# Performance work log

Measured on AMD Instinct MI355X. Metric: run time of the kernel, lower is better.

Reference implementation:

```python
import jax, jax.numpy as jnp
import numpy as np

B, C, N, K = 2, 128, 8192, 16
DL = 128  # dim_L; Fourier half-dim = 64; mlp hidden = 32


def setup_inputs() -> dict:
    key = jax.random.key(0)
    ks = jax.random.split(key, 16)
    s = 0.05
    return {
        "x": jax.random.normal(ks[0], (B, C, N, 1), jnp.float32),
        "coords": jax.random.normal(ks[1], (B, N, 4), jnp.float32),
        "idx": jax.random.randint(ks[2], (B, N, K), 0, N, jnp.int64),
        "B_gauss": jax.random.normal(ks[3], (4, DL // 2), jnp.float32),
        "W1": jax.random.normal(ks[4], (DL, DL // 4), jnp.float32) * s,
        "b1": jax.random.normal(ks[5], (DL // 4,), jnp.float32) * s,
        "W2": jax.random.normal(ks[6], (DL // 4, C), jnp.float32) * s,
        "b2": jax.random.normal(ks[7], (C,), jnp.float32) * s,
        "Wq": jax.random.normal(ks[8], (C, C), jnp.float32) * s,
        "bq": jax.random.normal(ks[9], (C,), jnp.float32) * s,
        "Wk": jax.random.normal(ks[10], (C, C), jnp.float32) * s,
        "bk": jax.random.normal(ks[11], (C,), jnp.float32) * s,
        "Wv": jax.random.normal(ks[12], (C, C), jnp.float32) * s,
        "bv": jax.random.normal(ks[13], (C,), jnp.float32) * s,
        "Wo": jax.random.normal(ks[14], (C, C), jnp.float32) * s,
        "bo": jax.random.normal(ks[15], (C,), jnp.float32) * s,
    }


def reference(x, coords, idx, B_gauss, W1, b1, W2, b2, Wq, bq, Wk, bk, Wv, bv, Wo, bo):
    xs = x[..., 0]  # [B, C, N]
    # gather neighbor coords/features via KNN idx (vmapped over batch)
    nb_coords = jax.vmap(lambda c, i: c[i])(coords, idx)          # [B, N, K, 4]
    nb_feats = jax.vmap(lambda f, i: f[:, i])(xs, idx)            # [B, C, N, K]
    delta_p = nb_coords - coords[:, :, None, :]                   # [B, N, K, 4]
    # random-Fourier geometric embedding
    proj = jnp.matmul(delta_p, B_gauss)                           # [B, N, K, DL/2]
    two_pi = 2.0 * jnp.pi
    E_freq = jnp.concatenate([jnp.sin(two_pi * proj), jnp.cos(two_pi * proj)], axis=-1)
    h = jax.nn.relu(E_freq @ W1 + b1) @ W2 + b2                   # [B, N, K, C]
    E_geo = jnp.transpose(h, (0, 3, 1, 2))                        # [B, C, N, K]
    # 1x1 conv projections == channel matmuls (PyTorch conv weight acts as out<-in)
    Q = jnp.einsum('oc,bcn->bon', Wq, xs) + bq[None, :, None]     # [B, C, N]
    KV_in = nb_feats + E_geo                                      # [B, C, N, K]
    Kt = jnp.einsum('oc,bcnk->bonk', Wk, KV_in) + bk[None, :, None, None]
    Vt = jnp.einsum('oc,bcnk->bonk', Wv, KV_in) + bv[None, :, None, None]
    # local dot-product attention over K neighbors
    attn = jnp.sum(Q[..., None] * Kt, axis=1, keepdims=True) / jnp.sqrt(jnp.float32(C))
    attn = jax.nn.softmax(attn, axis=-1)                          # [B, 1, N, K]
    out = jnp.sum(attn * Vt, axis=-1, keepdims=True)              # [B, C, N, 1]
    out = jnp.einsum('oc,bcnk->bonk', Wo, out) + bo[None, :, None, None]
    return out
```

## Files before the change

kernel.cpp:

```cpp
#include <hip/hip_runtime.h>


using u16 = unsigned short;
using u32 = unsigned int;
using u64 = unsigned long long;

typedef short bf16x8 __attribute__((ext_vector_type(8)));
typedef float f32x4  __attribute__((ext_vector_type(4)));

__device__ __forceinline__ float bl(u32 u) { return __uint_as_float(u << 16); }
__device__ __forceinline__ float bh(u32 u) { return __uint_as_float(u & 0xffff0000u); }
__device__ __forceinline__ float b2f(u16 u) { return __uint_as_float(((u32)u) << 16); }
__device__ __forceinline__ u16 f2b(float f) {
    u32 u = __float_as_uint(f);
    u32 r = u + 0x7fffu + ((u >> 16) & 1u);
    return (u16)(r >> 16);
}
__device__ __forceinline__ u64 pack4(float a, float b, float c, float d) {
    return (u64)f2b(a) | ((u64)f2b(b) << 16) | ((u64)f2b(c) << 32) | ((u64)f2b(d) << 48);
}
__device__ __forceinline__ int fidxA(int m, int c) {
    return (((m >> 4)*4 + (c >> 5))*64 + ((c >> 3) & 3)*16 + (m & 15))*8 + (c & 7);
}

__global__ void __launch_bounds__(512)
k_pt(const float* __restrict__ x,
     const float* __restrict__ Wq, const float* __restrict__ bq,
     const float* __restrict__ Wk,
     const float* __restrict__ Wv, const float* __restrict__ bv,
     const float* __restrict__ Wo, const float* __restrict__ bo,
     const float* __restrict__ W1, const float* __restrict__ W2,
     u16* __restrict__ Afrag, u16* __restrict__ Wovfrag,
     u16* __restrict__ W1frag, u16* __restrict__ W2frag,
     u16* __restrict__ Wow2frag,
     float* __restrict__ bA, float* __restrict__ bov,
     u16* __restrict__ xT)
{
    const int blk = blockIdx.x, tid = threadIdx.x;

    if (blk >= 130) {
        __shared__ u16 tile[32][33];
        const int blk2 = blk - 130;
        const int b  = blk2 >> 10;
        const int ct = (blk2 >> 8) & 3;
        const int nt = blk2 & 255;
        const int tx = tid & 31, ty = tid >> 5;
        const size_t xb = (size_t)b * 128 * 8192;
        #pragma unroll
        for (int j = 0; j < 2; ++j) {
            int c = ct*32 + ty + j*16;
            tile[ty + j*16][tx] = f2b(x[xb + (size_t)c * 8192 + (size_t)(nt*32 + tx)]);
        }
        __syncthreads();
        #pragma unroll
        for (int j = 0; j < 2; ++j) {
            int n = nt*32 + ty + j*16;
            xT[xb + (size_t)n * 128 + (size_t)(ct*32 + tx)] = tile[tx][ty + j*16];
        }
        return;
    }

    const int i = tid & 127, p = tid >> 7;
    if (blk < 128) {
        __shared__ float sWk[128], sWo[128];
        __shared__ float s_pA[4][128], s_pV[4][128];
        __shared__ float sWovRow[128];
        __shared__ float s_p2[32][17];
        if (tid < 128) sWk[tid] = Wk[tid*128 + blk];
        else if (tid < 256) sWo[tid-128] = Wo[blk*128 + (tid-128)];
        __syncthreads();
        float accA = 0.f, accV = 0.f;
        #pragma unroll 8
        for (int o = p*32; o < p*32 + 32; ++o) {
            accA += sWk[o] * Wq[o*128 + i];
            accV += sWo[o] * Wv[o*128 + i];
        }
        s_pA[p][i] = accA; s_pV[p][i] = accV;
        __syncthreads();
        if (tid < 128) {
            float v = s_pA[0][tid] + s_pA[1][tid] + s_pA[2][tid] + s_pA[3][tid];
            Afrag[fidxA(blk, tid)] = f2b(v);
        } else if (tid < 256) {
            int ii = tid - 128;
            float v = s_pV[0][ii] + s_pV[1][ii] + s_pV[2][ii] + s_pV[3][ii];
            Wovfrag[fidxA(blk, ii)] = f2b(v);
            sWovRow[ii] = v;
        }
        __syncthreads();
        {
            int h = tid >> 4, sub = tid & 15;
            float a = 0.f;
            #pragma unroll
            for (int jj = 0; jj < 8; ++jj)
                a += sWovRow[sub*8 + jj] * W2[h*128 + sub*8 + jj];
            s_p2[h][sub] = a;
        }
        __syncthreads();
        if (tid < 32) {
            float v = 0.f;
            #pragma unroll
            for (int s = 0; s < 16; ++s) v += s_p2[tid][s];
            Wow2frag[(((blk >> 4)*64 + (tid >> 3)*16 + (blk & 15)))*8 + (tid & 7)] = f2b(v);
        }
    } else if (blk == 128) {
        __shared__ float s_r[2][4][128];
        float a1 = 0.f, a3 = 0.f;
        #pragma unroll 8
        for (int o = p*32; o < p*32 + 32; ++o) {
            a1 += Wk[o*128 + i] * bq[o];
            a3 += Wo[i*128 + o] * bv[o];
        }
        s_r[0][p][i] = a1; s_r[1][p][i] = a3;
        __syncthreads();
        if (tid < 128) {
            bA[tid] = s_r[0][0][tid] + s_r[0][1][tid] + s_r[0][2][tid] + s_r[0][3][tid];
        } else if (tid < 256) {
            int ii = tid - 128;
            bov[ii] = s_r[1][0][ii] + s_r[1][1][ii] + s_r[1][2][ii] + s_r[1][3][ii] + bo[ii];
        }
    } else {
        for (int e = tid; e < 4096; e += 512) {
            int ii = e & 127, r2 = e >> 7;
            {
                int nt = r2 >> 4, lmm = r2 & 15;
                int ks = ii >> 5, q = (ii >> 3) & 3, j = ii & 7;
                W1frag[((nt*4 + ks)*64 + q*16 + lmm)*8 + j] = f2b(W1[ii*32 + r2]);
            }
            {
                int mt = r2 >> 4, lmm = r2 & 15;
                int ks = ii >> 5, q = (ii >> 3) & 3, j = ii & 7;
                W2frag[((mt*4 + ks)*64 + q*16 + lmm)*8 + j] = f2b(W2[r2*128 + ii]);
            }
        }
    }
}

__global__ void __launch_bounds__(256, 2)
k_main(const u16* __restrict__ xT, const float* __restrict__ coords,
       const int* __restrict__ idx, const float* __restrict__ Bg,
       const float* __restrict__ b1g, const float* __restrict__ b2g,
       const u16* __restrict__ Afrag, const u16* __restrict__ Wovfrag,
       const u16* __restrict__ W1frag, const u16* __restrict__ W2frag,
       const u16* __restrict__ Wow2frag,
       const float* __restrict__ bAg, const float* __restrict__ bovg,
       float* __restrict__ out)
{
    __shared__ __align__(16) u16   sH[128][40];
    __shared__ __align__(16) u16   s_qkb[8][136];
    __shared__ __align__(16) u16   s_gb[8][40];
    __shared__ __align__(16) u16   s_xbb[8][136];
    __shared__ __align__(16) float s_del[128][4];
    __shared__ float s_attn[8][17];
    __shared__ u16   sHbar[32][12];
    __shared__ __align__(16) float s_b2[128];
    __shared__ float s_bov[128], s_b1[32];
    __shared__ __align__(16) float sBgT[64][4];
    __shared__ int s_idx[128];

    const int tid = threadIdx.x;
    const int w = tid >> 6, l = tid & 63, lm = l & 15, lq = l >> 4, lmm = lm & 7;
    const int g0 = blockIdx.x * 8;
    const int bsel = g0 >> 13;
    const int n0 = g0 & 8191;
    const size_t bbase = ((size_t)bsel) << 13;
    const float inv_sqrtC = 0.08838834764831845f;

    if (tid < 128) { s_bov[tid] = bovg[tid]; s_b2[tid] = b2g[tid]; }
    else if (tid < 160) { s_b1[tid-128] = b1g[tid-128]; }
    sBgT[tid >> 2][tid & 3] = Bg[(tid & 3)*64 + (tid >> 2)];

    if (tid < 128) {
        int j = idx[(size_t)g0*16 + tid];
        s_idx[tid] = j;
        float4 cj = *(const float4*)&coords[(size_t)(bbase + j)*4];
        float4 cn = *(const float4*)&coords[(size_t)(g0 + (tid >> 4))*4];
        *(float4*)s_del[tid] = make_float4(cj.x-cn.x, cj.y-cn.y, cj.z-cn.z, cj.w-cn.w);
    }
    {
        f32x4 accq[2] = {{0.f,0.f,0.f,0.f},{0.f,0.f,0.f,0.f}};
        const bf16x8* Af = (const bf16x8*)Afrag;
        bf16x8 bfr[4];
        #pragma unroll
        for (int ks = 0; ks < 4; ++ks)
            bfr[ks] = *(const bf16x8*)&xT[(((size_t)(g0 + lmm)) << 7) + ks*32 + lq*8];
        #pragma unroll
        for (int mi = 0; mi < 2; ++mi) {
            const int ct = w*2 + mi;
            #pragma unroll
            for (int ks = 0; ks < 4; ++ks) {
                bf16x8 a = Af[(ct*4 + ks)*64 + l];
                accq[mi] = __builtin_amdgcn_mfma_f32_16x16x32_bf16(a, bfr[ks], accq[mi], 0, 0, 0);
            }
        }
        if (lm < 8) {
            #pragma unroll
            for (int mi = 0; mi < 2; ++mi) {
                int c0 = (w*2 + mi)*16 + lq*4;
                float4 ba4 = *(const float4*)&bAg[c0];
                *(u64*)&s_qkb[lm][c0] = pack4(accq[mi][0] + ba4.x, accq[mi][1] + ba4.y,
                                              accq[mi][2] + ba4.z, accq[mi][3] + ba4.w);
            }
        }
    }
    __syncthreads();

    {
        const bf16x8* W1f = (const bf16x8*)W1frag;
        bf16x8 w1f[2][4];
        #pragma unroll
        for (int nt = 0; nt < 2; ++nt)
            #pragma unroll
            for (int ks = 0; ks < 4; ++ks) w1f[nt][ks] = W1f[(nt*4 + ks)*64 + l];
        #pragma unroll
        for (int mi = 0; mi < 2; ++mi) {
            const int mt = w*2 + mi;
            float4 d = *(const float4*)s_del[mt*16 + lm];
            bf16x8 ea[4];
            #pragma unroll
            for (int ksp = 0; ksp < 2; ++ksp) {
                #pragma unroll
                for (int jp = 0; jp < 4; ++jp) {
                    int f = ksp*32 + lq*8 + jp*2;
                    float4 ga = *(const float4*)sBgT[f];
                    float4 gb = *(const float4*)sBgT[f+1];
                    float p0 = d.x*ga.x + d.y*ga.y + d.z*ga.z + d.w*ga.w;
                    float p1 = d.x*gb.x + d.y*gb.y + d.z*gb.z + d.w*gb.w;
                    p0 -= floorf(p0); p1 -= floorf(p1);
                    ((u32*)&ea[ksp])[jp]   = (u32)f2b(__builtin_amdgcn_sinf(p0))
                                           | ((u32)f2b(__builtin_amdgcn_sinf(p1)) << 16);
                    ((u32*)&ea[ksp+2])[jp] = (u32)f2b(__builtin_amdgcn_cosf(p0))
                                           | ((u32)f2b(__builtin_amdgcn_cosf(p1)) << 16);
                }
            }
            f32x4 acch[2] = {{0.f,0.f,0.f,0.f},{0.f,0.f,0.f,0.f}};
            #pragma unroll
            for (int ks = 0; ks < 4; ++ks) {
                acch[0] = __builtin_amdgcn_mfma_f32_16x16x32_bf16(ea[ks], w1f[0][ks], acch[0], 0,0,0);
                acch[1] = __builtin_amdgcn_mfma_f32_16x16x32_bf16(ea[ks], w1f[1][ks], acch[1], 0,0,0);
            }
            #pragma unroll
            for (int nt = 0; nt < 2; ++nt) {
                float b1v = s_b1[nt*16 + lm];
                #pragma unroll
                for (int r = 0; r < 4; ++r)
                    sH[mt*16 + lq*4 + r][nt*16 + lm] = f2b(fmaxf(acch[nt][r] + b1v, 0.f));
            }
        }
    }
    if (w < 2) {
        const bf16x8* W2f = (const bf16x8*)W2frag;
        f32x4 accg = {0.f,0.f,0.f,0.f};
        #pragma unroll
        for (int ks = 0; ks < 4; ++ks) {
            bf16x8 a = W2f[(w*4 + ks)*64 + l];
            bf16x8 bv = *(const bf16x8*)&s_qkb[lmm][ks*32 + lq*8];
            accg = __builtin_amdgcn_mfma_f32_16x16x32_bf16(a, bv, accg, 0, 0, 0);
        }
        if (lm < 8) {
            int m0 = w*16 + lq*4;
            *(u64*)&s_gb[lm][m0] = pack4(accg[0], accg[1], accg[2], accg[3]);
        }
    }
    __syncthreads();

    {
        bf16x8 xnb[2][4];
        const size_t rb0 = ((size_t)(bbase + s_idx[(w*2 + 0)*16 + lm])) << 7;
        const size_t rb1 = ((size_t)(bbase + s_idx[(w*2 + 1)*16 + lm])) << 7;
        #pragma unroll
        for (int ks = 0; ks < 4; ++ks)
            xnb[0][ks] = *(const bf16x8*)&xT[rb0 + ks*32 + lq*8];
        #pragma unroll
        for (int ks = 0; ks < 4; ++ks)
            xnb[1][ks] = *(const bf16x8*)&xT[rb1 + ks*32 + lq*8];
        bf16x8 bq4[5];
        #pragma unroll
        for (int ks = 0; ks < 4; ++ks) bq4[ks] = *(const bf16x8*)&s_qkb[lmm][ks*32 + lq*8];
        bq4[4] = *(const bf16x8*)&s_gb[lmm][lq*8];
        #pragma unroll
        for (int mi = 0; mi < 2; ++mi) {
            const int mt = w*2 + mi;
            f32x4 acc = {0.f,0.f,0.f,0.f};
            #pragma unroll
            for (int ks = 0; ks < 4; ++ks)
                acc = __builtin_amdgcn_mfma_f32_16x16x32_bf16(xnb[mi][ks], bq4[ks], acc, 0, 0, 0);
            {
                bf16x8 a = *(const bf16x8*)&sH[mt*16 + lm][lq*8];
                acc = __builtin_amdgcn_mfma_f32_16x16x32_bf16(a, bq4[4], acc, 0, 0, 0);
            }
            float s0 = acc[0]*inv_sqrtC, s1 = acc[1]*inv_sqrtC;
            float s2 = acc[2]*inv_sqrtC, s3 = acc[3]*inv_sqrtC;
            float mx = fmaxf(fmaxf(s0, s1), fmaxf(s2, s3));
            mx = fmaxf(mx, __shfl_xor(mx, 16));
            mx = fmaxf(mx, __shfl_xor(mx, 32));
            float e0 = __expf(s0 - mx), e1 = __expf(s1 - mx);
            float e2 = __expf(s2 - mx), e3 = __expf(s3 - mx);
            float sm = (e0 + e1) + (e2 + e3);
            sm += __shfl_xor(sm, 16);
            sm += __shfl_xor(sm, 32);
            if (lm == mt) {
                float inv = 1.0f / sm;
                s_attn[mt][lq*4 + 0] = e0*inv;
                s_attn[mt][lq*4 + 1] = e1*inv;
                s_attn[mt][lq*4 + 2] = e2*inv;
                s_attn[mt][lq*4 + 3] = e3*inv;
            }
        }
    }
    __syncthreads();

    if (tid < 128) {
        int n = tid >> 4, cs = tid & 15, c0 = cs*8;
        float a0[16];
        #pragma unroll
        for (int k = 0; k < 16; ++k) a0[k] = s_attn[n][k];
        float4 f0 = *(const float4*)&s_b2[c0];
        float4 f1 = *(const float4*)&s_b2[c0+4];
        #pragma unroll
        for (int k = 0; k < 16; ++k) {
            uint4 v = *(const uint4*)&xT[(((size_t)(bbase + s_idx[n*16 + k])) << 7) + c0];
            f0.x += a0[k]*bl(v.x); f0.y += a0[k]*bh(v.x);
            f0.z += a0[k]*bl(v.y); f0.w += a0[k]*bh(v.y);
            f1.x += a0[k]*bl(v.z); f1.y += a0[k]*bh(v.z);
            f1.z += a0[k]*bl(v.w); f1.w += a0[k]*bh(v.w);
        }
        *(u64*)&s_xbb[n][c0]   = pack4(f0.x, f0.y, f0.z, f0.w);
        *(u64*)&s_xbb[n][c0+4] = pack4(f1.x, f1.y, f1.z, f1.w);
    } else {
        int t = tid - 128;
        int n = t >> 4, m0 = (t & 15)*2;
        float h0 = 0.f, h1 = 0.f;
        #pragma unroll
        for (int k = 0; k < 16; ++k) {
            float ak = s_attn[n][k];
            u32 hv = *(const u32*)&sH[n*16 + k][m0];
            h0 += ak * bl(hv);
            h1 += ak * bh(hv);
        }
        sHbar[m0][n]   = f2b(h0);
        sHbar[m0+1][n] = f2b(h1);
    }
    __syncthreads();

    {
        const bf16x8* Wvf = (const bf16x8*)Wovfrag;
        const bf16x8* W2f = (const bf16x8*)Wow2frag;
        bf16x8 bv[4];
        #pragma unroll
        for (int ks = 0; ks < 4; ++ks) bv[ks] = *(const bf16x8*)&s_xbb[lmm][ks*32 + lq*8];
        bf16x8 bvh;
        #pragma unroll
        for (int j = 0; j < 8; ++j) bvh[j] = (short)sHbar[lq*8 + j][lmm];
        #pragma unroll
        for (int mi = 0; mi < 2; ++mi) {
            const int ct = w*2 + mi;
            f32x4 acco = {0.f,0.f,0.f,0.f};
            acco = __builtin_amdgcn_mfma_f32_16x16x32_bf16(W2f[ct*64 + l], bvh, acco, 0, 0, 0);
            #pragma unroll
            for (int ks = 0; ks < 4; ++ks) {
                bf16x8 a = Wvf[(ct*4 + ks)*64 + l];
                acco = __builtin_amdgcn_mfma_f32_16x16x32_bf16(a, bv[ks], acco, 0, 0, 0);
            }
            if (lm < 8) {
                #pragma unroll
                for (int r = 0; r < 4; ++r) {
                    int o = ct*16 + lq*4 + r;
                    out[(((size_t)(bsel*128 + o)) << 13) + n0 + lm] = acco[r] + s_bov[o];
                }
            }
        }
    }
}

extern "C" void kernel_launch(void* const* d_in, const int* in_sizes, int n_in,
                              void* d_out, int out_size, void* d_ws, size_t ws_size,
                              hipStream_t stream)
{
    const float* x      = (const float*)d_in[0];
    const float* coords = (const float*)d_in[1];
    const int*   idx    = (const int*)d_in[2];
    const float* Bg     = (const float*)d_in[3];
    const float* W1     = (const float*)d_in[4];
    const float* b1     = (const float*)d_in[5];
    const float* W2     = (const float*)d_in[6];
    const float* b2     = (const float*)d_in[7];
    const float* Wq     = (const float*)d_in[8];
    const float* bq     = (const float*)d_in[9];
    const float* Wk     = (const float*)d_in[10];
    const float* bk     = (const float*)d_in[11];
    const float* Wv     = (const float*)d_in[12];
    const float* bv     = (const float*)d_in[13];
    const float* Wo     = (const float*)d_in[14];
    const float* bo     = (const float*)d_in[15];
    float* out = (float*)d_out;
    (void)bk;

    char* ws = (char*)d_ws;
    u16*   Afrag    = (u16*)(ws);
    u16*   Wovfrag  = (u16*)(ws + 32768);
    u16*   W1frag   = (u16*)(ws + 65536);
    u16*   W2frag   = (u16*)(ws + 73728);
    u16*   Wow2frag = (u16*)(ws + 81920);
    float* bA       = (float*)(ws + 90112);
    float* bov      = (float*)(ws + 90624);
    u16*   xT       = (u16*)(ws + 94208);

    k_pt<<<2178, 512, 0, stream>>>(x, Wq, bq, Wk, Wv, bv, Wo, bo, W1, W2,
                                   Afrag, Wovfrag, W1frag, W2frag, Wow2frag,
                                   bA, bov, xT);
    k_main<<<2048, 256, 0, stream>>>(xT, coords, idx, Bg, b1, b2,
                                     Afrag, Wovfrag, W1frag, W2frag, Wow2frag,
                                     bA, bov, out);
}
```

Measured before the change: 131.0 us.

## Process 16 points per block to fill MFMA tiles instead of 8

Each block now handles 16 query points instead of 8, so every 16x16 MFMA uses all 16 N-columns rather than discarding half of them (the lm<8 masks and lmm aliasing go away). Per-block loops over neighbor tiles double, shared arrays are resized, and the two previously split thread halves now each do both the feature and hidden-state attention reductions. This halves the grid and amortizes weight-fragment loads across twice as many points, at the cost of more LDS per block, more work per thread, and fewer blocks for latency hiding.

```diff
diff --git a/kernel.cpp b/kernel.cpp
--- a/kernel.cpp
+++ b/kernel.cpp
@@ -145,21 +145,21 @@
        const float* __restrict__ bAg, const float* __restrict__ bovg,
        float* __restrict__ out)
 {
-    __shared__ __align__(16) u16   sH[128][40];
-    __shared__ __align__(16) u16   s_qkb[8][136];
-    __shared__ __align__(16) u16   s_gb[8][40];
-    __shared__ __align__(16) u16   s_xbb[8][136];
-    __shared__ __align__(16) float s_del[128][4];
-    __shared__ float s_attn[8][17];
-    __shared__ u16   sHbar[32][12];
+    __shared__ __align__(16) u16   sH[256][40];
+    __shared__ __align__(16) u16   s_qkb[16][136];
+    __shared__ __align__(16) u16   s_gb[16][40];
+    __shared__ __align__(16) u16   s_xbb[16][136];
+    __shared__ __align__(16) float s_del[256][4];
+    __shared__ float s_attn[16][17];
+    __shared__ u16   sHbar[32][18];
     __shared__ __align__(16) float s_b2[128];
     __shared__ float s_bov[128], s_b1[32];
     __shared__ __align__(16) float sBgT[64][4];
-    __shared__ int s_idx[128];
+    __shared__ int s_idx[256];
 
     const int tid = threadIdx.x;
-    const int w = tid >> 6, l = tid & 63, lm = l & 15, lq = l >> 4, lmm = lm & 7;
-    const int g0 = blockIdx.x * 8;
+    const int w = tid >> 6, l = tid & 63, lm = l & 15, lq = l >> 4;
+    const int g0 = blockIdx.x * 16;
     const int bsel = g0 >> 13;
     const int n0 = g0 & 8191;
     const size_t bbase = ((size_t)bsel) << 13;
@@ -169,7 +169,7 @@
     else if (tid < 160) { s_b1[tid-128] = b1g[tid-128]; }
     sBgT[tid >> 2][tid & 3] = Bg[(tid & 3)*64 + (tid >> 2)];
 
-    if (tid < 128) {
+    {
         int j = idx[(size_t)g0*16 + tid];
         s_idx[tid] = j;
         float4 cj = *(const float4*)&coords[(size_t)(bbase + j)*4];
@@ -182,7 +182,7 @@
         bf16x8 bfr[4];
         #pragma unroll
         for (int ks = 0; ks < 4; ++ks)
-            bfr[ks] = *(const bf16x8*)&xT[(((size_t)(g0 + lmm)) << 7) + ks*32 + lq*8];
+            bfr[ks] = *(const bf16x8*)&xT[(((size_t)(g0 + lm)) << 7) + ks*32 + lq*8];
         #pragma unroll
         for (int mi = 0; mi < 2; ++mi) {
             const int ct = w*2 + mi;
@@ -192,14 +192,12 @@
                 accq[mi] = __builtin_amdgcn_mfma_f32_16x16x32_bf16(a, bfr[ks], accq[mi], 0, 0, 0);
             }
         }
-        if (lm < 8) {
-            #pragma unroll
-            for (int mi = 0; mi < 2; ++mi) {
-                int c0 = (w*2 + mi)*16 + lq*4;
-                float4 ba4 = *(const float4*)&bAg[c0];
-                *(u64*)&s_qkb[lm][c0] = pack4(accq[mi][0] + ba4.x, accq[mi][1] + ba4.y,
-                                              accq[mi][2] + ba4.z, accq[mi][3] + ba4.w);
-            }
+        #pragma unroll
+        for (int mi = 0; mi < 2; ++mi) {
+            int c0 = (w*2 + mi)*16 + lq*4;
+            float4 ba4 = *(const float4*)&bAg[c0];
+            *(u64*)&s_qkb[lm][c0] = pack4(accq[mi][0] + ba4.x, accq[mi][1] + ba4.y,
+                                          accq[mi][2] + ba4.z, accq[mi][3] + ba4.w);
         }
     }
     __syncthreads();
@@ -212,8 +210,8 @@
             #pragma unroll
             for (int ks = 0; ks < 4; ++ks) w1f[nt][ks] = W1f[(nt*4 + ks)*64 + l];
         #pragma unroll
-        for (int mi = 0; mi < 2; ++mi) {
-            const int mt = w*2 + mi;
+        for (int mi = 0; mi < 4; ++mi) {
+            const int mt = w*4 + mi;
             float4 d = *(const float4*)s_del[mt*16 + lm];
             bf16x8 ea[4];
             #pragma unroll
@@ -253,10 +251,10 @@
         #pragma unroll
         for (int ks = 0; ks < 4; ++ks) {
             bf16x8 a = W2f[(w*4 + ks)*64 + l];
-            bf16x8 bv = *(const bf16x8*)&s_qkb[lmm][ks*32 + lq*8];
+            bf16x8 bv = *(const bf16x8*)&s_qkb[lm][ks*32 + lq*8];
             accg = __builtin_amdgcn_mfma_f32_16x16x32_bf16(a, bv, accg, 0, 0, 0);
         }
-        if (lm < 8) {
+        {
             int m0 = w*16 + lq*4;
             *(u64*)&s_gb[lm][m0] = pack4(accg[0], accg[1], accg[2], accg[3]);
         }
@@ -264,26 +262,22 @@
     __syncthreads();
 
     {
-        bf16x8 xnb[2][4];
-        const size_t rb0 = ((size_t)(bbase + s_idx[(w*2 + 0)*16 + lm])) << 7;
-        const size_t rb1 = ((size_t)(bbase + s_idx[(w*2 + 1)*16 + lm])) << 7;
-        #pragma unroll
-        for (int ks = 0; ks < 4; ++ks)
-            xnb[0][ks] = *(const bf16x8*)&xT[rb0 + ks*32 + lq*8];
-        #pragma unroll
-        for (int ks = 0; ks < 4; ++ks)
-            xnb[1][ks] = *(const bf16x8*)&xT[rb1 + ks*32 + lq*8];
         bf16x8 bq4[5];
         #pragma unroll
-        for (int ks = 0; ks < 4; ++ks) bq4[ks] = *(const bf16x8*)&s_qkb[lmm][ks*32 + lq*8];
-        bq4[4] = *(const bf16x8*)&s_gb[lmm][lq*8];
-        #pragma unroll
-        for (int mi = 0; mi < 2; ++mi) {
-            const int mt = w*2 + mi;
+        for (int ks = 0; ks < 4; ++ks) bq4[ks] = *(const bf16x8*)&s_qkb[lm][ks*32 + lq*8];
+        bq4[4] = *(const bf16x8*)&s_gb[lm][lq*8];
+        #pragma unroll
+        for (int mi = 0; mi < 4; ++mi) {
+            const int mt = w*4 + mi;
+            bf16x8 xnb[4];
+            const size_t rb = ((size_t)(bbase + s_idx[mt*16 + lm])) << 7;
+            #pragma unroll
+            for (int ks = 0; ks < 4; ++ks)
+                xnb[ks] = *(const bf16x8*)&xT[rb + ks*32 + lq*8];
             f32x4 acc = {0.f,0.f,0.f,0.f};
             #pragma unroll
             for (int ks = 0; ks < 4; ++ks)
-                acc = __builtin_amdgcn_mfma_f32_16x16x32_bf16(xnb[mi][ks], bq4[ks], acc, 0, 0, 0);
+                acc = __builtin_amdgcn_mfma_f32_16x16x32_bf16(xnb[ks], bq4[ks], acc, 0, 0, 0);
             {
                 bf16x8 a = *(const bf16x8*)&sH[mt*16 + lm][lq*8];
                 acc = __builtin_amdgcn_mfma_f32_16x16x32_bf16(a, bq4[4], acc, 0, 0, 0);
@@ -309,7 +303,7 @@
     }
     __syncthreads();
 
-    if (tid < 128) {
+    {
         int n = tid >> 4, cs = tid & 15, c0 = cs*8;
         float a0[16];
         #pragma unroll
@@ -326,13 +320,11 @@
         }
         *(u64*)&s_xbb[n][c0]   = pack4(f0.x, f0.y, f0.z, f0.w);
         *(u64*)&s_xbb[n][c0+4] = pack4(f1.x, f1.y, f1.z, f1.w);
-    } else {
-        int t = tid - 128;
-        int n = t >> 4, m0 = (t & 15)*2;
+        int m0 = cs*2;
         float h0 = 0.f, h1 = 0.f;
         #pragma unroll
         for (int k = 0; k < 16; ++k) {
-            float ak = s_attn[n][k];
+            float ak = a0[k];
             u32 hv = *(const u32*)&sH[n*16 + k][m0];
             h0 += ak * bl(hv);
             h1 += ak * bh(hv);
@@ -347,10 +339,10 @@
         const bf16x8* W2f = (const bf16x8*)Wow2frag;
         bf16x8 bv[4];
         #pragma unroll
-        for (int ks = 0; ks < 4; ++ks) bv[ks] = *(const bf16x8*)&s_xbb[lmm][ks*32 + lq*8];
+        for (int ks = 0; ks < 4; ++ks) bv[ks] = *(const bf16x8*)&s_xbb[lm][ks*32 + lq*8];
         bf16x8 bvh;
         #pragma unroll
-        for (int j = 0; j < 8; ++j) bvh[j] = (short)sHbar[lq*8 + j][lmm];
+        for (int j = 0; j < 8; ++j) bvh[j] = (short)sHbar[lq*8 + j][lm];
         #pragma unroll
         for (int mi = 0; mi < 2; ++mi) {
             const int ct = w*2 + mi;
@@ -361,12 +353,10 @@
                 bf16x8 a = Wvf[(ct*4 + ks)*64 + l];
                 acco = __builtin_amdgcn_mfma_f32_16x16x32_bf16(a, bv[ks], acco, 0, 0, 0);
             }
-            if (lm < 8) {
-                #pragma unroll
-                for (int r = 0; r < 4; ++r) {
-                    int o = ct*16 + lq*4 + r;
-                    out[(((size_t)(bsel*128 + o)) << 13) + n0 + lm] = acco[r] + s_bov[o];
-                }
+            #pragma unroll
+            for (int r = 0; r < 4; ++r) {
+                int o = ct*16 + lq*4 + r;
+                out[(((size_t)(bsel*128 + o)) << 13) + n0 + lm] = acco[r] + s_bov[o];
             }
         }
     }
@@ -408,7 +398,7 @@
     k_pt<<<2178, 512, 0, stream>>>(x, Wq, bq, Wk, Wv, bv, Wo, bo, W1, W2,
                                    Afrag, Wovfrag, W1frag, W2frag, Wow2frag,
                                    bA, bov, xT);
-    k_main<<<2048, 256, 0, stream>>>(xT, coords, idx, Bg, b1, b2,
+    k_main<<<1024, 256, 0, stream>>>(xT, coords, idx, Bg, b1, b2,
                                      Afrag, Wovfrag, W1frag, W2frag, Wow2frag,
                                      bA, bov, out);
 }
```

Result: faster. 123.6 us (-5.6%).
